# Optimization experiments

Measured on AMD Instinct MI355X. Metric: run time of the kernel, lower is better.

## Reference

```python
import jax, jax.numpy as jnp
import numpy as np

N_EXPERTS = 8
D_MODEL = 1024
D_FF = 4096


def setup_inputs() -> dict:
    key = jax.random.key(0)
    k_x, k_idx, k_g, k_u, k_d = jax.random.split(key, 5)
    scale_in = 1.0 / np.sqrt(D_MODEL)
    scale_ff = 1.0 / np.sqrt(D_FF)
    return {
        "x": jax.random.normal(k_x, (2, 1024, D_MODEL), dtype=jnp.float32),
        "expert_idx": jax.random.randint(k_idx, (2, 1024), 0, N_EXPERTS, dtype=jnp.int64),
        "w_gate": jax.random.normal(k_g, (N_EXPERTS, D_MODEL, D_FF), dtype=jnp.float32) * scale_in,
        "w_up": jax.random.normal(k_u, (N_EXPERTS, D_MODEL, D_FF), dtype=jnp.float32) * scale_in,
        "w_down": jax.random.normal(k_d, (N_EXPERTS, D_FF, D_MODEL), dtype=jnp.float32) * scale_ff,
    }


def reference(x, expert_idx, w_gate, w_up, w_down):
    # x: [B, S, D]; expert_idx: [B, S] in [0, N_EXPERTS)
    B, S, D = x.shape
    x_flat = x.reshape(-1, D)                  # [T, D]
    idx_flat = expert_idx.reshape(-1)          # [T]
    out = jnp.zeros_like(x_flat)
    # Faithful per-expert dispatch: each token is processed by exactly one
    # expert's SwiGLU FFN; masked scatter-back combines results.
    for e in range(N_EXPERTS):
        mask = (idx_flat == e)[:, None]        # [T, 1]
        gate = jax.nn.silu(x_flat @ w_gate[e]) # [T, F]
        up = x_flat @ w_up[e]                  # [T, F]
        y = (gate * up) @ w_down[e]            # [T, D]
        out = jnp.where(mask, y, out)
    return out.reshape(B, S, D)
```

## Files before the change

kernel.cpp:

```cpp
#include <hip/hip_runtime.h>
#include <hip/hip_bf16.h>
#include <stdint.h>

#define N_EXPERTS 8
#define D_MODEL   1024
#define D_FF      4096
#define T_TOKENS  2048
#define MT        128
#define MAXT      24
#define KSPLIT    4

typedef __attribute__((ext_vector_type(8))) short bf16x8;
typedef __attribute__((ext_vector_type(4))) float f32x4;

#define XG_OFF   (16384)
#define H_OFF    (16384 + 4u*1024*1024)
#define WG_OFF   (32u*1024*1024)
#define WU_OFF   (96u*1024*1024)
#define WD_OFF   (160u*1024*1024)

__device__ __forceinline__ unsigned short f2bfu(float f) {
    union { float f; uint32_t u; } v; v.f = f;
    uint32_t u = v.u;
    return (unsigned short)((u + 0x7fffu + ((u >> 16) & 1u)) >> 16);
}

__device__ __forceinline__ short f2bf(float f) { return (short)f2bfu(f); }

__device__ __forceinline__ uint32_t pack2bf(float a, float b) {
    __hip_bfloat162 h = __float22bfloat162_rn(make_float2(a, b));
    return *(uint32_t*)&h;
}

__device__ __forceinline__ void gl_lds16(const short* g, short* l) {
    __builtin_amdgcn_global_load_lds(
        (const __attribute__((address_space(1))) unsigned int*)(g),
        (__attribute__((address_space(3))) unsigned int*)(l), 16, 0, 0);
}


__global__ void moe_route(const int* __restrict__ idx, int* __restrict__ offsets,
                          int* __restrict__ ntp, int* __restrict__ t_e,
                          int* __restrict__ t_p0, int* __restrict__ t_end) {
    __shared__ int cnt[N_EXPERTS];
    int tid = threadIdx.x;
    if (tid < N_EXPERTS) cnt[tid] = 0;
    __syncthreads();
    for (int t = tid; t < T_TOKENS; t += 256) atomicAdd(&cnt[idx[t]], 1);
    __syncthreads();
    if (tid == 0) {
        int off = 0, nt = 0;
        for (int e = 0; e < N_EXPERTS; ++e) {
            offsets[e] = off;
            int c = cnt[e], end = off + c;
            for (int i = 0; i < c; i += MT) { t_e[nt] = e; t_p0[nt] = off + i; t_end[nt] = end; ++nt; }
            off = end;
        }
        offsets[N_EXPERTS] = off;
        *ntp = nt;
    }
}

__global__ void moe_gather(const float* __restrict__ x, const int* __restrict__ idx,
                           const int* __restrict__ offsets, int* __restrict__ cursor,
                           int* __restrict__ tok_of_row, short* __restrict__ Xg) {
    __shared__ int sp;
    int t = blockIdx.x;
    if (threadIdx.x == 0) {
        int e = idx[t];
        int p = offsets[e] + atomicAdd(&cursor[e], 1);
        tok_of_row[p] = t;
        sp = p;
    }
    __syncthreads();
    int p = sp;
    const float4* src = (const float4*)(x + (size_t)t * D_MODEL);
    uint2* dst = (uint2*)(Xg + (size_t)p * D_MODEL);
    int i = threadIdx.x;
    float4 v = src[i];
    uint2 o;
    o.x = pack2bf(v.x, v.y);
    o.y = pack2bf(v.z, v.w);
    dst[i] = o;
}


__launch_bounds__(256)
__global__ void moe_repack(const float* __restrict__ src, short* __restrict__ dst,
                           int K, int N) {
    __shared__ short Lt[256][72];

    int e = blockIdx.z, kslab = blockIdx.y, nslab = blockIdx.x;
    int NT = N >> 6, KS = K >> 6;
    int tid = threadIdx.x;
    int w = tid >> 6, l = tid & 63;

    const float* sb = src + ((size_t)e * K + (size_t)kslab * 64) * N
                      + (size_t)nslab * 256 + 4 * l;

#pragma unroll
    for (int g = 0; g < 4; ++g) {
        int r0 = g * 16 + w * 4;
        float4 v0 = *(const float4*)(sb + (size_t)(r0    ) * N);
        float4 v1 = *(const float4*)(sb + (size_t)(r0 + 1) * N);
        float4 v2 = *(const float4*)(sb + (size_t)(r0 + 2) * N);
        float4 v3 = *(const float4*)(sb + (size_t)(r0 + 3) * N);
        {
            int n = 4 * l + 0; int cc = r0 ^ (((n >> 3) & 3) << 3);
            ushort4 tv = { f2bfu(v0.x), f2bfu(v1.x), f2bfu(v2.x), f2bfu(v3.x) };
            *(ushort4*)&Lt[n][cc] = tv;
        }
        {
            int n = 4 * l + 1; int cc = r0 ^ (((n >> 3) & 3) << 3);
            ushort4 tv = { f2bfu(v0.y), f2bfu(v1.y), f2bfu(v2.y), f2bfu(v3.y) };
            *(ushort4*)&Lt[n][cc] = tv;
        }
        {
            int n = 4 * l + 2; int cc = r0 ^ (((n >> 3) & 3) << 3);
            ushort4 tv = { f2bfu(v0.z), f2bfu(v1.z), f2bfu(v2.z), f2bfu(v3.z) };
            *(ushort4*)&Lt[n][cc] = tv;
        }
        {
            int n = 4 * l + 3; int cc = r0 ^ (((n >> 3) & 3) << 3);
            ushort4 tv = { f2bfu(v0.w), f2bfu(v1.w), f2bfu(v2.w), f2bfu(v3.w) };
            *(ushort4*)&Lt[n][cc] = tv;
        }
    }
    __syncthreads();

    int t = tid >> 6, idx = tid & 63;
#pragma unroll
    for (int i = 0; i < 8; ++i) {
        int u = i * 64 + idx;
        int n = u >> 3, k8 = u & 7;
        int sw = ((n >> 3) & 3) << 3;
        bf16x8 vv = *(const bf16x8*)&Lt[t * 64 + n][(k8 * 8) ^ sw];
        size_t tb = (((size_t)e * NT + (size_t)nslab * 4 + t) * KS + kslab) * 4096;
        *(bf16x8*)&dst[tb + n * 64 + ((k8 ^ (n & 7)) * 8)] = vv;
    }
}


__launch_bounds__(256)
__global__ void moe_gemm1(const short* __restrict__ wgt, const short* __restrict__ wut,
                          const short* __restrict__ Xg, short* __restrict__ h,
                          const int* __restrict__ t_e, const int* __restrict__ t_p0,
                          const int* __restrict__ t_end, const int* __restrict__ ntp) {
    int ti = blockIdx.y;
    if (ti >= *ntp) return;
    int e = t_e[ti], p0 = t_p0[ti], pend = t_end[ti];
    int nt = blockIdx.x;

    __shared__ short Bg[2][4096];
    __shared__ short Bu[2][4096];

    int tid = threadIdx.x;
    int lane = tid & 63, w = tid >> 6;
    int col = lane & 15, quad = lane >> 4;

    const short* gsrc = wgt + ((size_t)e * 64 + nt) * 16 * 4096 + w * 1024 + lane * 8;
    const short* usrc = wut + ((size_t)e * 64 + nt) * 16 * 4096 + w * 1024 + lane * 8;

    int row0 = p0 + w * 32 + col;  if (row0 > T_TOKENS - 1) row0 = T_TOKENS - 1;
    int row1 = row0 + 16;          if (row1 > T_TOKENS - 1) row1 = T_TOKENS - 1;
    const short* a0p = Xg + (size_t)row0 * D_MODEL + quad * 8;
    const short* a1p = Xg + (size_t)row1 * D_MODEL + quad * 8;

    int boff0[4], boff1[4];
#pragma unroll
    for (int nf = 0; nf < 4; ++nf) {
        int n = nf * 16 + col;
        boff0[nf] = n * 64 + ((quad ^ (n & 7)) * 8);
        boff1[nf] = n * 64 + (((quad + 4) ^ (n & 7)) * 8);
    }

    f32x4 accg[2][4], accu[2][4];
#pragma unroll
    for (int m = 0; m < 2; ++m)
#pragma unroll
        for (int nf = 0; nf < 4; ++nf) {
            accg[m][nf] = (f32x4){0,0,0,0};
            accu[m][nf] = (f32x4){0,0,0,0};
        }

    gl_lds16(gsrc,       &Bg[0][w * 1024]);
    gl_lds16(gsrc + 512, &Bg[0][w * 1024 + 512]);
    gl_lds16(usrc,       &Bu[0][w * 1024]);
    gl_lds16(usrc + 512, &Bu[0][w * 1024 + 512]);
    bf16x8 a00 = *(const bf16x8*)(a0p);
    bf16x8 a01 = *(const bf16x8*)(a0p + 32);
    bf16x8 a10 = *(const bf16x8*)(a1p);
    bf16x8 a11 = *(const bf16x8*)(a1p + 32);
    __syncthreads();

    int p = 0;
#pragma unroll 1
    for (int it = 0; it < 16; ++it) {
        int itn = (it + 1) & 15;
        const short* gs = gsrc + (size_t)itn * 4096;
        const short* us = usrc + (size_t)itn * 4096;
        gl_lds16(gs,       &Bg[p ^ 1][w * 1024]);
        gl_lds16(gs + 512, &Bg[p ^ 1][w * 1024 + 512]);
        gl_lds16(us,       &Bu[p ^ 1][w * 1024]);
        gl_lds16(us + 512, &Bu[p ^ 1][w * 1024 + 512]);
        int kn = itn * 64;
        bf16x8 a00n = *(const bf16x8*)(a0p + kn);
        bf16x8 a01n = *(const bf16x8*)(a0p + kn + 32);
        bf16x8 a10n = *(const bf16x8*)(a1p + kn);
        bf16x8 a11n = *(const bf16x8*)(a1p + kn + 32);

#pragma unroll
        for (int nf = 0; nf < 4; ++nf) {
            bf16x8 bg0 = *(const bf16x8*)&Bg[p][boff0[nf]];
            bf16x8 bg1 = *(const bf16x8*)&Bg[p][boff1[nf]];
            bf16x8 bu0 = *(const bf16x8*)&Bu[p][boff0[nf]];
            bf16x8 bu1 = *(const bf16x8*)&Bu[p][boff1[nf]];
            accg[0][nf] = __builtin_amdgcn_mfma_f32_16x16x32_bf16(a00, bg0, accg[0][nf], 0, 0, 0);
            accg[0][nf] = __builtin_amdgcn_mfma_f32_16x16x32_bf16(a01, bg1, accg[0][nf], 0, 0, 0);
            accg[1][nf] = __builtin_amdgcn_mfma_f32_16x16x32_bf16(a10, bg0, accg[1][nf], 0, 0, 0);
            accg[1][nf] = __builtin_amdgcn_mfma_f32_16x16x32_bf16(a11, bg1, accg[1][nf], 0, 0, 0);
            accu[0][nf] = __builtin_amdgcn_mfma_f32_16x16x32_bf16(a00, bu0, accu[0][nf], 0, 0, 0);
            accu[0][nf] = __builtin_amdgcn_mfma_f32_16x16x32_bf16(a01, bu1, accu[0][nf], 0, 0, 0);
            accu[1][nf] = __builtin_amdgcn_mfma_f32_16x16x32_bf16(a10, bu0, accu[1][nf], 0, 0, 0);
            accu[1][nf] = __builtin_amdgcn_mfma_f32_16x16x32_bf16(a11, bu1, accu[1][nf], 0, 0, 0);
        }

        a00 = a00n; a01 = a01n; a10 = a10n; a11 = a11n;
        __syncthreads();
        p ^= 1;
    }

#pragma unroll
    for (int m = 0; m < 2; ++m) {
#pragma unroll
        for (int r = 0; r < 4; ++r) {
            int mr = p0 + w * 32 + m * 16 + quad * 4 + r;
            if (mr < pend) {
#pragma unroll
                for (int nf = 0; nf < 4; ++nf) {
                    float gv = accg[m][nf][r], uv = accu[m][nf][r];
                    float hv = (gv / (1.f + __expf(-gv))) * uv;
                    h[(size_t)mr * D_FF + nt * 64 + nf * 16 + col] = f2bf(hv);
                }
            }
        }
    }
}


__launch_bounds__(256)
__global__ void moe_gemm2(const short* __restrict__ wdt, const short* __restrict__ h,
                          const int* __restrict__ tok_of_row, float* __restrict__ out,
                          const int* __restrict__ t_e, const int* __restrict__ t_p0,
                          const int* __restrict__ t_end, const int* __restrict__ ntp) {
    int ti = blockIdx.y;
    if (ti >= *ntp) return;
    int e = t_e[ti], p0 = t_p0[ti], pend = t_end[ti];
    int dt = blockIdx.x, z = blockIdx.z;

    __shared__ short Bd[2][4096];

    int tid = threadIdx.x;
    int lane = tid & 63, w = tid >> 6;
    int col = lane & 15, quad = lane >> 4;

    const short* dsrc = wdt + (((size_t)e * 16 + dt) * 64 + z * 16) * 4096 + w * 1024 + lane * 8;
    int Koff = z * (D_FF / KSPLIT);

    int row0 = p0 + w * 32 + col;  if (row0 > T_TOKENS - 1) row0 = T_TOKENS - 1;
    int row1 = row0 + 16;          if (row1 > T_TOKENS - 1) row1 = T_TOKENS - 1;
    const short* a0p = h + (size_t)row0 * D_FF + Koff + quad * 8;
    const short* a1p = h + (size_t)row1 * D_FF + Koff + quad * 8;

    int boff0[4], boff1[4];
#pragma unroll
    for (int nf = 0; nf < 4; ++nf) {
        int n = nf * 16 + col;
        boff0[nf] = n * 64 + ((quad ^ (n & 7)) * 8);
        boff1[nf] = n * 64 + (((quad + 4) ^ (n & 7)) * 8);
    }

    f32x4 acc[2][4];
#pragma unroll
    for (int m = 0; m < 2; ++m)
#pragma unroll
        for (int nf = 0; nf < 4; ++nf) acc[m][nf] = (f32x4){0,0,0,0};

    gl_lds16(dsrc,       &Bd[0][w * 1024]);
    gl_lds16(dsrc + 512, &Bd[0][w * 1024 + 512]);
    bf16x8 a00 = *(const bf16x8*)(a0p);
    bf16x8 a01 = *(const bf16x8*)(a0p + 32);
    bf16x8 a10 = *(const bf16x8*)(a1p);
    bf16x8 a11 = *(const bf16x8*)(a1p + 32);
    __syncthreads();

    int p = 0;
#pragma unroll 1
    for (int it = 0; it < 16; ++it) {
        int itn = (it + 1) & 15;
        const short* ds = dsrc + (size_t)itn * 4096;
        gl_lds16(ds,       &Bd[p ^ 1][w * 1024]);
        gl_lds16(ds + 512, &Bd[p ^ 1][w * 1024 + 512]);
        int kn = itn * 64;
        bf16x8 a00n = *(const bf16x8*)(a0p + kn);
        bf16x8 a01n = *(const bf16x8*)(a0p + kn + 32);
        bf16x8 a10n = *(const bf16x8*)(a1p + kn);
        bf16x8 a11n = *(const bf16x8*)(a1p + kn + 32);

#pragma unroll
        for (int nf = 0; nf < 4; ++nf) {
            bf16x8 b0 = *(const bf16x8*)&Bd[p][boff0[nf]];
            bf16x8 b1 = *(const bf16x8*)&Bd[p][boff1[nf]];
            acc[0][nf] = __builtin_amdgcn_mfma_f32_16x16x32_bf16(a00, b0, acc[0][nf], 0, 0, 0);
            acc[0][nf] = __builtin_amdgcn_mfma_f32_16x16x32_bf16(a01, b1, acc[0][nf], 0, 0, 0);
            acc[1][nf] = __builtin_amdgcn_mfma_f32_16x16x32_bf16(a10, b0, acc[1][nf], 0, 0, 0);
            acc[1][nf] = __builtin_amdgcn_mfma_f32_16x16x32_bf16(a11, b1, acc[1][nf], 0, 0, 0);
        }

        a00 = a00n; a01 = a01n; a10 = a10n; a11 = a11n;
        __syncthreads();
        p ^= 1;
    }

#pragma unroll
    for (int m = 0; m < 2; ++m) {
#pragma unroll
        for (int r = 0; r < 4; ++r) {
            int mr = p0 + w * 32 + m * 16 + quad * 4 + r;
            if (mr < pend) {
                int t = tok_of_row[mr];
#pragma unroll
                for (int nf = 0; nf < 4; ++nf)
                    atomicAdd(&out[(size_t)t * D_MODEL + dt * 64 + nf * 16 + col], acc[m][nf][r]);
            }
        }
    }
}


extern "C" void kernel_launch(void* const* d_in, const int* in_sizes, int n_in,
                              void* d_out, int out_size, void* d_ws, size_t ws_size,
                              hipStream_t stream) {
    (void)in_sizes; (void)n_in; (void)out_size; (void)ws_size;
    const float* x   = (const float*)d_in[0];
    const int*   idx = (const int*)d_in[1];
    const float* wg  = (const float*)d_in[2];
    const float* wu  = (const float*)d_in[3];
    const float* wd  = (const float*)d_in[4];
    float* out = (float*)d_out;

    int* ws_i       = (int*)d_ws;
    int* cursor     = ws_i;
    int* offsets    = ws_i + 8;
    int* nt         = ws_i + 20;
    int* t_e        = ws_i + 32;
    int* t_p0       = ws_i + 64;
    int* t_end      = ws_i + 96;
    int* tok_of_row = ws_i + 256;

    short* Xg  = (short*)((char*)d_ws + XG_OFF);
    short* h   = (short*)((char*)d_ws + H_OFF);
    short* WGt = (short*)((char*)d_ws + WG_OFF);
    short* WUt = (short*)((char*)d_ws + WU_OFF);
    short* WDt = (short*)((char*)d_ws + WD_OFF);

    hipMemsetAsync(d_ws, 0, 128, stream);
    hipMemsetAsync(out, 0, (size_t)T_TOKENS * D_MODEL * sizeof(float), stream);
    moe_route<<<dim3(1), 256, 0, stream>>>(idx, offsets, nt, t_e, t_p0, t_end);
    moe_gather<<<dim3(T_TOKENS), 256, 0, stream>>>(x, idx, offsets, cursor, tok_of_row, Xg);
    moe_repack<<<dim3(D_FF / 256, D_MODEL / 64, N_EXPERTS), 256, 0, stream>>>(wg, WGt, D_MODEL, D_FF);
    moe_repack<<<dim3(D_FF / 256, D_MODEL / 64, N_EXPERTS), 256, 0, stream>>>(wu, WUt, D_MODEL, D_FF);
    moe_repack<<<dim3(D_MODEL / 256, D_FF / 64, N_EXPERTS), 256, 0, stream>>>(wd, WDt, D_FF, D_MODEL);
    moe_gemm1<<<dim3(D_FF / 64, MAXT), 256, 0, stream>>>(WGt, WUt, Xg, h,
                                                         t_e, t_p0, t_end, nt);
    moe_gemm2<<<dim3(D_MODEL / 64, MAXT, KSPLIT), 256, 0, stream>>>(WDt, h, tok_of_row, out,
                                                                    t_e, t_p0, t_end, nt);
}
```

Baseline: 605.5 us.

## Triple-buffer GEMM weight loads with partial vmcnt waits and widen repack blocks

```diff
diff --git a/kernel.cpp b/kernel.cpp
--- a/kernel.cpp
+++ b/kernel.cpp
@@ -37,6 +37,12 @@
         (const __attribute__((address_space(1))) unsigned int*)(g),
         (__attribute__((address_space(3))) unsigned int*)(l), 16, 0, 0);
 }
+
+#define PIPE_BARRIER(N)                                              \
+    asm volatile("s_waitcnt vmcnt(" #N ") lgkmcnt(0)" ::: "memory"); \
+    __builtin_amdgcn_sched_barrier(0);                               \
+    __builtin_amdgcn_s_barrier();                                    \
+    __builtin_amdgcn_sched_barrier(0);
 
 
 __global__ void moe_route(const int* __restrict__ idx, int* __restrict__ offsets,
@@ -85,57 +91,60 @@
 }
 
 
-__launch_bounds__(256)
+__launch_bounds__(512)
 __global__ void moe_repack(const float* __restrict__ src, short* __restrict__ dst,
                            int K, int N) {
-    __shared__ short Lt[256][72];
-
-    int e = blockIdx.z, kslab = blockIdx.y, nslab = blockIdx.x;
+    __shared__ short Lt[512][72];
+
+    int e = blockIdx.z, ks = blockIdx.y, nc = blockIdx.x;
     int NT = N >> 6, KS = K >> 6;
     int tid = threadIdx.x;
     int w = tid >> 6, l = tid & 63;
 
-    const float* sb = src + ((size_t)e * K + (size_t)kslab * 64) * N
-                      + (size_t)nslab * 256 + 4 * l;
-
-#pragma unroll
-    for (int g = 0; g < 4; ++g) {
-        int r0 = g * 16 + w * 4;
-        float4 v0 = *(const float4*)(sb + (size_t)(r0    ) * N);
-        float4 v1 = *(const float4*)(sb + (size_t)(r0 + 1) * N);
-        float4 v2 = *(const float4*)(sb + (size_t)(r0 + 2) * N);
-        float4 v3 = *(const float4*)(sb + (size_t)(r0 + 3) * N);
-        {
-            int n = 4 * l + 0; int cc = r0 ^ (((n >> 3) & 3) << 3);
-            ushort4 tv = { f2bfu(v0.x), f2bfu(v1.x), f2bfu(v2.x), f2bfu(v3.x) };
-            *(ushort4*)&Lt[n][cc] = tv;
-        }
-        {
-            int n = 4 * l + 1; int cc = r0 ^ (((n >> 3) & 3) << 3);
-            ushort4 tv = { f2bfu(v0.y), f2bfu(v1.y), f2bfu(v2.y), f2bfu(v3.y) };
-            *(ushort4*)&Lt[n][cc] = tv;
-        }
-        {
-            int n = 4 * l + 2; int cc = r0 ^ (((n >> 3) & 3) << 3);
-            ushort4 tv = { f2bfu(v0.z), f2bfu(v1.z), f2bfu(v2.z), f2bfu(v3.z) };
-            *(ushort4*)&Lt[n][cc] = tv;
-        }
-        {
-            int n = 4 * l + 3; int cc = r0 ^ (((n >> 3) & 3) << 3);
-            ushort4 tv = { f2bfu(v0.w), f2bfu(v1.w), f2bfu(v2.w), f2bfu(v3.w) };
-            *(ushort4*)&Lt[n][cc] = tv;
+    const float* sb = src + ((size_t)e * K + (size_t)ks * 64 + w * 8) * N + (size_t)nc * 512;
+
+#pragma unroll
+    for (int q = 0; q < 2; ++q) {
+        int r0 = w * 8 + q * 4;
+#pragma unroll
+        for (int hc = 0; hc < 2; ++hc) {
+            int c = 4 * l + hc * 256;
+            float4 v0 = *(const float4*)(sb + ((size_t)(q * 4 + 0)) * N + c);
+            float4 v1 = *(const float4*)(sb + ((size_t)(q * 4 + 1)) * N + c);
+            float4 v2 = *(const float4*)(sb + ((size_t)(q * 4 + 2)) * N + c);
+            float4 v3 = *(const float4*)(sb + ((size_t)(q * 4 + 3)) * N + c);
+            {
+                int n = c + 0; int cc = r0 ^ (((n >> 3) & 3) << 3);
+                ushort4 tv = { f2bfu(v0.x), f2bfu(v1.x), f2bfu(v2.x), f2bfu(v3.x) };
+                *(ushort4*)&Lt[n][cc] = tv;
+            }
+            {
+                int n = c + 1; int cc = r0 ^ (((n >> 3) & 3) << 3);
+                ushort4 tv = { f2bfu(v0.y), f2bfu(v1.y), f2bfu(v2.y), f2bfu(v3.y) };
+                *(ushort4*)&Lt[n][cc] = tv;
+            }
+            {
+                int n = c + 2; int cc = r0 ^ (((n >> 3) & 3) << 3);
+                ushort4 tv = { f2bfu(v0.z), f2bfu(v1.z), f2bfu(v2.z), f2bfu(v3.z) };
+                *(ushort4*)&Lt[n][cc] = tv;
+            }
+            {
+                int n = c + 3; int cc = r0 ^ (((n >> 3) & 3) << 3);
+                ushort4 tv = { f2bfu(v0.w), f2bfu(v1.w), f2bfu(v2.w), f2bfu(v3.w) };
+                *(ushort4*)&Lt[n][cc] = tv;
+            }
         }
     }
     __syncthreads();
 
-    int t = tid >> 6, idx = tid & 63;
+    int t = w;
+    size_t tb = (((size_t)e * NT + (size_t)nc * 8 + t) * KS + ks) * 4096;
 #pragma unroll
     for (int i = 0; i < 8; ++i) {
-        int u = i * 64 + idx;
+        int u = i * 64 + l;
         int n = u >> 3, k8 = u & 7;
         int sw = ((n >> 3) & 3) << 3;
         bf16x8 vv = *(const bf16x8*)&Lt[t * 64 + n][(k8 * 8) ^ sw];
-        size_t tb = (((size_t)e * NT + (size_t)nslab * 4 + t) * KS + kslab) * 4096;
         *(bf16x8*)&dst[tb + n * 64 + ((k8 ^ (n & 7)) * 8)] = vv;
     }
 }
@@ -151,8 +160,8 @@
     int e = t_e[ti], p0 = t_p0[ti], pend = t_end[ti];
     int nt = blockIdx.x;
 
-    __shared__ short Bg[2][4096];
-    __shared__ short Bu[2][4096];
+    __shared__ short Bg[3][4096];
+    __shared__ short Bu[3][4096];
 
     int tid = threadIdx.x;
     int lane = tid & 63, w = tid >> 6;
@@ -183,38 +192,52 @@
             accu[m][nf] = (f32x4){0,0,0,0};
         }
 
-    gl_lds16(gsrc,       &Bg[0][w * 1024]);
-    gl_lds16(gsrc + 512, &Bg[0][w * 1024 + 512]);
-    gl_lds16(usrc,       &Bu[0][w * 1024]);
-    gl_lds16(usrc + 512, &Bu[0][w * 1024 + 512]);
-    bf16x8 a00 = *(const bf16x8*)(a0p);
-    bf16x8 a01 = *(const bf16x8*)(a0p + 32);
-    bf16x8 a10 = *(const bf16x8*)(a1p);
-    bf16x8 a11 = *(const bf16x8*)(a1p + 32);
-    __syncthreads();
-
-    int p = 0;
-#pragma unroll 1
+    bf16x8 a[2][4];
+
+    gl_lds16(gsrc,        &Bg[0][w * 1024]);
+    gl_lds16(gsrc + 512,  &Bg[0][w * 1024 + 512]);
+    gl_lds16(usrc,        &Bu[0][w * 1024]);
+    gl_lds16(usrc + 512,  &Bu[0][w * 1024 + 512]);
+    gl_lds16(gsrc + 4096,       &Bg[1][w * 1024]);
+    gl_lds16(gsrc + 4096 + 512, &Bg[1][w * 1024 + 512]);
+    gl_lds16(usrc + 4096,       &Bu[1][w * 1024]);
+    gl_lds16(usrc + 4096 + 512, &Bu[1][w * 1024 + 512]);
+    a[0][0] = *(const bf16x8*)(a0p);
+    a[0][1] = *(const bf16x8*)(a0p + 32);
+    a[0][2] = *(const bf16x8*)(a1p);
+    a[0][3] = *(const bf16x8*)(a1p + 32);
+    PIPE_BARRIER(8)
+
+#pragma unroll
     for (int it = 0; it < 16; ++it) {
-        int itn = (it + 1) & 15;
-        const short* gs = gsrc + (size_t)itn * 4096;
-        const short* us = usrc + (size_t)itn * 4096;
-        gl_lds16(gs,       &Bg[p ^ 1][w * 1024]);
-        gl_lds16(gs + 512, &Bg[p ^ 1][w * 1024 + 512]);
-        gl_lds16(us,       &Bu[p ^ 1][w * 1024]);
-        gl_lds16(us + 512, &Bu[p ^ 1][w * 1024 + 512]);
-        int kn = itn * 64;
-        bf16x8 a00n = *(const bf16x8*)(a0p + kn);
-        bf16x8 a01n = *(const bf16x8*)(a0p + kn + 32);
-        bf16x8 a10n = *(const bf16x8*)(a1p + kn);
-        bf16x8 a11n = *(const bf16x8*)(a1p + kn + 32);
-
+        if (it + 2 < 16) {
+            const short* gs = gsrc + (size_t)(it + 2) * 4096;
+            const short* us = usrc + (size_t)(it + 2) * 4096;
+            short* bg = &Bg[(it + 2) % 3][w * 1024];
+            short* bu = &Bu[(it + 2) % 3][w * 1024];
+            gl_lds16(gs,       bg);
+            gl_lds16(gs + 512, bg + 512);
+            gl_lds16(us,       bu);
+            gl_lds16(us + 512, bu + 512);
+        }
+        if (it + 1 < 16) {
+            int kn = (it + 1) * 64;
+            a[(it + 1) & 1][0] = *(const bf16x8*)(a0p + kn);
+            a[(it + 1) & 1][1] = *(const bf16x8*)(a0p + kn + 32);
+            a[(it + 1) & 1][2] = *(const bf16x8*)(a1p + kn);
+            a[(it + 1) & 1][3] = *(const bf16x8*)(a1p + kn + 32);
+        }
+
+        const short* Bgb = &Bg[it % 3][0];
+        const short* Bub = &Bu[it % 3][0];
+        bf16x8 a00 = a[it & 1][0], a01 = a[it & 1][1];
+        bf16x8 a10 = a[it & 1][2], a11 = a[it & 1][3];
 #pragma unroll
         for (int nf = 0; nf < 4; ++nf) {
-            bf16x8 bg0 = *(const bf16x8*)&Bg[p][boff0[nf]];
-            bf16x8 bg1 = *(const bf16x8*)&Bg[p][boff1[nf]];
-            bf16x8 bu0 = *(const bf16x8*)&Bu[p][boff0[nf]];
-            bf16x8 bu1 = *(const bf16x8*)&Bu[p][boff1[nf]];
+            bf16x8 bg0 = *(const bf16x8*)&Bgb[boff0[nf]];
+            bf16x8 bg1 = *(const bf16x8*)&Bgb[boff1[nf]];
+            bf16x8 bu0 = *(const bf16x8*)&Bub[boff0[nf]];
+            bf16x8 bu1 = *(const bf16x8*)&Bub[boff1[nf]];
             accg[0][nf] = __builtin_amdgcn_mfma_f32_16x16x32_bf16(a00, bg0, accg[0][nf], 0, 0, 0);
             accg[0][nf] = __builtin_amdgcn_mfma_f32_16x16x32_bf16(a01, bg1, accg[0][nf], 0, 0, 0);
             accg[1][nf] = __builtin_amdgcn_mfma_f32_16x16x32_bf16(a10, bg0, accg[1][nf], 0, 0, 0);
@@ -225,9 +248,11 @@
             accu[1][nf] = __builtin_amdgcn_mfma_f32_16x16x32_bf16(a11, bu1, accu[1][nf], 0, 0, 0);
         }
 
-        a00 = a00n; a01 = a01n; a10 = a10n; a11 = a11n;
-        __syncthreads();
-        p ^= 1;
+        if (it < 14) {
+            PIPE_BARRIER(8)
+        } else if (it < 15) {
+            PIPE_BARRIER(4)
+        }
     }
 
 #pragma unroll
@@ -258,7 +283,7 @@
     int e = t_e[ti], p0 = t_p0[ti], pend = t_end[ti];
     int dt = blockIdx.x, z = blockIdx.z;
 
-    __shared__ short Bd[2][4096];
+    __shared__ short Bd[3][4096];
 
     int tid = threadIdx.x;
     int lane = tid & 63, w = tid >> 6;
@@ -286,40 +311,52 @@
 #pragma unroll
         for (int nf = 0; nf < 4; ++nf) acc[m][nf] = (f32x4){0,0,0,0};
 
-    gl_lds16(dsrc,       &Bd[0][w * 1024]);
-    gl_lds16(dsrc + 512, &Bd[0][w * 1024 + 512]);
-    bf16x8 a00 = *(const bf16x8*)(a0p);
-    bf16x8 a01 = *(const bf16x8*)(a0p + 32);
-    bf16x8 a10 = *(const bf16x8*)(a1p);
-    bf16x8 a11 = *(const bf16x8*)(a1p + 32);
-    __syncthreads();
-
-    int p = 0;
-#pragma unroll 1
+    bf16x8 a[2][4];
+
+    gl_lds16(dsrc,              &Bd[0][w * 1024]);
+    gl_lds16(dsrc + 512,        &Bd[0][w * 1024 + 512]);
+    gl_lds16(dsrc + 4096,       &Bd[1][w * 1024]);
+    gl_lds16(dsrc + 4096 + 512, &Bd[1][w * 1024 + 512]);
+    a[0][0] = *(const bf16x8*)(a0p);
+    a[0][1] = *(const bf16x8*)(a0p + 32);
+    a[0][2] = *(const bf16x8*)(a1p);
+    a[0][3] = *(const bf16x8*)(a1p + 32);
+    PIPE_BARRIER(6)
+
+#pragma unroll
     for (int it = 0; it < 16; ++it) {
-        int itn = (it + 1) & 15;
-        const short* ds = dsrc + (size_t)itn * 4096;
-        gl_lds16(ds,       &Bd[p ^ 1][w * 1024]);
-        gl_lds16(ds + 512, &Bd[p ^ 1][w * 1024 + 512]);
-        int kn = itn * 64;
-        bf16x8 a00n = *(const bf16x8*)(a0p + kn);
-        bf16x8 a01n = *(const bf16x8*)(a0p + kn + 32);
-        bf16x8 a10n = *(const bf16x8*)(a1p + kn);
-        bf16x8 a11n = *(const bf16x8*)(a1p + kn + 32);
-
+        if (it + 2 < 16) {
+            const short* ds = dsrc + (size_t)(it + 2) * 4096;
+            short* bd = &Bd[(it + 2) % 3][w * 1024];
+            gl_lds16(ds,       bd);
+            gl_lds16(ds + 512, bd + 512);
+        }
+        if (it + 1 < 16) {
+            int kn = (it + 1) * 64;
+            a[(it + 1) & 1][0] = *(const bf16x8*)(a0p + kn);
+            a[(it + 1) & 1][1] = *(const bf16x8*)(a0p + kn + 32);
+            a[(it + 1) & 1][2] = *(const bf16x8*)(a1p + kn);
+            a[(it + 1) & 1][3] = *(const bf16x8*)(a1p + kn + 32);
+        }
+
+        const short* Bdb = &Bd[it % 3][0];
+        bf16x8 a00 = a[it & 1][0], a01 = a[it & 1][1];
+        bf16x8 a10 = a[it & 1][2], a11 = a[it & 1][3];
 #pragma unroll
         for (int nf = 0; nf < 4; ++nf) {
-            bf16x8 b0 = *(const bf16x8*)&Bd[p][boff0[nf]];
-            bf16x8 b1 = *(const bf16x8*)&Bd[p][boff1[nf]];
+            bf16x8 b0 = *(const bf16x8*)&Bdb[boff0[nf]];
+            bf16x8 b1 = *(const bf16x8*)&Bdb[boff1[nf]];
             acc[0][nf] = __builtin_amdgcn_mfma_f32_16x16x32_bf16(a00, b0, acc[0][nf], 0, 0, 0);
             acc[0][nf] = __builtin_amdgcn_mfma_f32_16x16x32_bf16(a01, b1, acc[0][nf], 0, 0, 0);
             acc[1][nf] = __builtin_amdgcn_mfma_f32_16x16x32_bf16(a10, b0, acc[1][nf], 0, 0, 0);
             acc[1][nf] = __builtin_amdgcn_mfma_f32_16x16x32_bf16(a11, b1, acc[1][nf], 0, 0, 0);
         }
 
-        a00 = a00n; a01 = a01n; a10 = a10n; a11 = a11n;
-        __syncthreads();
-        p ^= 1;
+        if (it < 14) {
+            PIPE_BARRIER(6)
+        } else if (it < 15) {
+            PIPE_BARRIER(4)
+        }
     }
 
 #pragma unroll
@@ -368,9 +405,9 @@
     hipMemsetAsync(out, 0, (size_t)T_TOKENS * D_MODEL * sizeof(float), stream);
     moe_route<<<dim3(1), 256, 0, stream>>>(idx, offsets, nt, t_e, t_p0, t_end);
     moe_gather<<<dim3(T_TOKENS), 256, 0, stream>>>(x, idx, offsets, cursor, tok_of_row, Xg);
-    moe_repack<<<dim3(D_FF / 256, D_MODEL / 64, N_EXPERTS), 256, 0, stream>>>(wg, WGt, D_MODEL, D_FF);
-    moe_repack<<<dim3(D_FF / 256, D_MODEL / 64, N_EXPERTS), 256, 0, stream>>>(wu, WUt, D_MODEL, D_FF);
-    moe_repack<<<dim3(D_MODEL / 256, D_FF / 64, N_EXPERTS), 256, 0, stream>>>(wd, WDt, D_FF, D_MODEL);
+    moe_repack<<<dim3(D_FF / 512, D_MODEL / 64, N_EXPERTS), 512, 0, stream>>>(wg, WGt, D_MODEL, D_FF);
+    moe_repack<<<dim3(D_FF / 512, D_MODEL / 64, N_EXPERTS), 512, 0, stream>>>(wu, WUt, D_MODEL, D_FF);
+    moe_repack<<<dim3(D_MODEL / 512, D_FF / 64, N_EXPERTS), 512, 0, stream>>>(wd, WDt, D_FF, D_MODEL);
     moe_gemm1<<<dim3(D_FF / 64, MAXT), 256, 0, stream>>>(WGt, WUt, Xg, h,
                                                          t_e, t_p0, t_end, nt);
     moe_gemm2<<<dim3(D_MODEL / 64, MAXT, KSPLIT), 256, 0, stream>>>(WDt, h, tok_of_row, out,
```

Result: faster. 566.7 us (-6.4%).
